# Performance work log

Hardware: AMD Instinct MI355X
Metric: run time of the kernel (lower is better)

Reference implementation:

```python
import math
import jax, jax.numpy as jnp
import numpy as np

N_HEADS, INPUT_DIM, EMBED_DIM = 8, 512, 512
KEY_DIM = EMBED_DIM // N_HEADS  # 64, val_dim == key_dim
BATCH, N = 4, 2048


def setup_inputs() -> dict:
    key = jax.random.key(0)
    ks = jax.random.split(key, 6)
    def unif(k, shape):
        stdv = 1.0 / math.sqrt(shape[-1])
        return jax.random.uniform(k, shape, jnp.float32, -stdv, stdv)
    q = jax.random.normal(ks[0], (BATCH, N, INPUT_DIM), jnp.float32)
    mask = jax.random.randint(ks[1], (BATCH, N, N), 0, 2, jnp.int32)
    W_query = unif(ks[2], (N_HEADS, INPUT_DIM, KEY_DIM))
    W_key = unif(ks[3], (N_HEADS, INPUT_DIM, KEY_DIM))
    W_val = unif(ks[4], (N_HEADS, INPUT_DIM, KEY_DIM))
    W_out = unif(ks[5], (N_HEADS, KEY_DIM, EMBED_DIM))
    return {"q": q, "mask": mask, "W_query": W_query, "W_key": W_key,
            "W_val": W_val, "W_out": W_out}


def reference(q, mask, W_query, W_key, W_val, W_out):
    # Self-attention: k is None, v is None -> k = q, v = q (module forward_).
    norm = 1.0 / math.sqrt(KEY_DIM)
    m = mask.astype(bool)[None]  # (1, b, nq, ng) broadcast over heads
    Q = jnp.einsum('bnd,hdk->hbnk', q, W_query)  # (h, b, nq, dk)
    K = jnp.einsum('bnd,hdk->hbnk', q, W_key)    # (h, b, ng, dk)
    V = jnp.einsum('bnd,hdv->hbnv', q, W_val)    # (h, b, ng, dv)
    scores = norm * jnp.einsum('hbqk,hbgk->hbqg', Q, K)  # (h, b, nq, ng)
    scores = jnp.where(m, -jnp.inf, scores)
    attn = jax.nn.softmax(scores, axis=-1)
    attn = jnp.where(m, 0.0, attn)  # zero out masked (also kills NaN rows)
    heads = jnp.einsum('hbqg,hbgv->hbqv', attn, V)
    out = jnp.einsum('hbqv,hve->bqe', heads, W_out)  # (b, nq, embed)
    return out
```

## Files before the change

### kernel.cpp

```cpp
#include <hip/hip_runtime.h>
#include <hip/hip_bf16.h>
#include <stdint.h>

using bf16 = __hip_bfloat16;
typedef __attribute__((ext_vector_type(8))) short short8;
typedef __attribute__((ext_vector_type(4))) short short4b;
typedef __attribute__((ext_vector_type(4))) float f32x4;
typedef __attribute__((ext_vector_type(4))) unsigned int u32x4;

#if __has_builtin(__builtin_amdgcn_exp2f)
#define EXP2(x) __builtin_amdgcn_exp2f(x)
#else
#define EXP2(x) exp2f(x)
#endif

__device__ __forceinline__ short8 load8(const bf16* p) {
  return *reinterpret_cast<const short8*>(p);
}
__device__ __forceinline__ short f2b(float f) {
  return __builtin_bit_cast(short, __float2bfloat16(f));
}
__device__ __forceinline__ unsigned int cvtpk(float lo, float hi) {
  unsigned int r;
  asm("v_cvt_pk_bf16_f32 %0, %1, %2" : "=v"(r) : "v"(lo), "v"(hi));
  return r;
}
__device__ __forceinline__ void asy16(const bf16* g, bf16* l) {
  __builtin_amdgcn_global_load_lds(
      (const __attribute__((address_space(1))) void*)g,
      (__attribute__((address_space(3))) void*)l, 16, 0, 0);
}


__global__ void k_prep(const float4* __restrict__ x, ushort4* __restrict__ xb,
                       const float* __restrict__ Wq, const float* __restrict__ Wk,
                       const float* __restrict__ Wv, const float* __restrict__ Wo,
                       bf16* __restrict__ Wcat, bf16* __restrict__ Wot,
                       const int4* __restrict__ m4,
                       unsigned long long* __restrict__ bits) {
  int blk = blockIdx.x;
  const int tid = threadIdx.x;
  if (blk < 4096) {
    int i = blk * 256 + tid;
    float4 v = x[i];
    ushort4 o;
    o.x = (unsigned short)f2b(v.x);
    o.y = (unsigned short)f2b(v.y);
    o.z = (unsigned short)f2b(v.z);
    o.w = (unsigned short)f2b(v.w);
    xb[i] = o;
  } else if (blk < 4352) {
    int t = blk - 4096;
    __shared__ float T[64][65];
    if (t < 192) {
      int which = t >> 6;
      int h = (t >> 3) & 7, dt = t & 7;
      const float* W = (which == 0) ? Wq : ((which == 1) ? Wk : Wv);
#pragma unroll
      for (int p = 0; p < 4; ++p) {
        int row = p * 16 + (tid >> 4);
        float4 v = *(const float4*)(W + (size_t)(h * 512 + dt * 64 + row) * 64 +
                                    (tid & 15) * 4);
        T[row][(tid & 15) * 4 + 0] = v.x;
        T[row][(tid & 15) * 4 + 1] = v.y;
        T[row][(tid & 15) * 4 + 2] = v.z;
        T[row][(tid & 15) * 4 + 3] = v.w;
      }
      __syncthreads();
      float scale = (which == 0) ? 0.18033688011112042f : 1.0f;
      int jj = tid >> 2, i0 = (tid & 3) * 16;
#pragma unroll
      for (int q = 0; q < 2; ++q) {
        short8 o;
#pragma unroll
        for (int e = 0; e < 8; ++e) o[e] = f2b(T[i0 + q * 8 + e][jj] * scale);
        *(short8*)(Wcat + (size_t)(which * 512 + h * 64 + jj) * 512 + dt * 64 +
                   i0 + q * 8) = o;
      }
    } else {
      int t2 = t - 192;
      int h = t2 >> 3, et = t2 & 7;
#pragma unroll
      for (int p = 0; p < 4; ++p) {
        int row = p * 16 + (tid >> 4);
        float4 v = *(const float4*)(Wo + (size_t)(h * 64 + row) * 512 + et * 64 +
                                    (tid & 15) * 4);
        T[row][(tid & 15) * 4 + 0] = v.x;
        T[row][(tid & 15) * 4 + 1] = v.y;
        T[row][(tid & 15) * 4 + 2] = v.z;
        T[row][(tid & 15) * 4 + 3] = v.w;
      }
      __syncthreads();
      int jj = tid >> 2, i0 = (tid & 3) * 16;
#pragma unroll
      for (int q = 0; q < 2; ++q) {
        short8 o;
#pragma unroll
        for (int e = 0; e < 8; ++e) o[e] = f2b(T[i0 + q * 8 + e][jj]);
        *(short8*)(Wot + (size_t)(et * 64 + jj) * 512 + h * 64 + i0 + q * 8) = o;
      }
    }
  } else {
    int i = (blk - 4352) * 256 + tid;
    int4 v = m4[i];
    unsigned int nib = (unsigned)(v.x != 0) | ((unsigned)(v.y != 0) << 1) |
                       ((unsigned)(v.z != 0) << 2) | ((unsigned)(v.w != 0) << 3);
    unsigned long long w = (unsigned long long)nib << (4 * (tid & 15));
    w |= __shfl_xor(w, 1);
    w |= __shfl_xor(w, 2);
    w |= __shfl_xor(w, 4);
    w |= __shfl_xor(w, 8);
    if ((tid & 15) == 0) bits[i >> 4] = w;
  }
}

__device__ __forceinline__ void gemm128(const bf16* __restrict__ A,
                                        const bf16* __restrict__ Bt,
                                        bf16* As, bf16* Bs,
                                        int rowBase, int colBase,
                                        f32x4 acc[4][4]) {
  const int tid = threadIdx.x;
  const int lane = tid & 63, w = tid >> 6;
  const int g = lane >> 4, r = lane & 15;

  auto stage = [&](int buf, int s) {
#pragma unroll
    for (int p = 0; p < 2; ++p) {
      int c = p * 256 + tid;
      int row = c >> 2, gr = c & 3, sg = gr ^ (row & 3);
      asy16(A + (size_t)(rowBase + row) * 512 + s * 32 + sg * 8,
            As + buf * 4096 + c * 8);
    }
#pragma unroll
    for (int p = 0; p < 2; ++p) {
      int c = p * 256 + tid;
      int row = c >> 2, gr = c & 3, sg = gr ^ (row & 3);
      asy16(Bt + (size_t)(colBase + row) * 512 + s * 32 + sg * 8,
            Bs + buf * 4096 + c * 8);
    }
  };

  stage(0, 0);
  int buf = 0;
  const int rbl = (w >> 1) * 64, cbl = (w & 1) * 64;
  for (int s = 0; s < 16; ++s) {
    __syncthreads();
    if (s < 15) stage(buf ^ 1, s + 1);
    const bf16* a0 = As + buf * 4096;
    const bf16* b0 = Bs + buf * 4096;
    short8 af[4], bfr[4];
#pragma unroll
    for (int mt = 0; mt < 4; ++mt) {
      int row = rbl + mt * 16 + r;
      af[mt] = load8(a0 + (row * 4 + (g ^ (row & 3))) * 8);
    }
#pragma unroll
    for (int nt = 0; nt < 4; ++nt) {
      int col = cbl + nt * 16 + r;
      bfr[nt] = load8(b0 + (col * 4 + (g ^ (col & 3))) * 8);
    }
#pragma unroll
    for (int mt = 0; mt < 4; ++mt)
#pragma unroll
      for (int nt = 0; nt < 4; ++nt)
        acc[mt][nt] = __builtin_amdgcn_mfma_f32_16x16x32_bf16(
            af[mt], bfr[nt], acc[mt][nt], 0, 0, 0);
    buf ^= 1;
  }
}

__device__ __forceinline__ void gemm64x128(const bf16* __restrict__ A,
                                           const bf16* __restrict__ Bt,
                                           bf16* As, bf16* Bs,
                                           int rowBase, int colBase,
                                           f32x4 acc[2][4]) {
  const int tid = threadIdx.x;
  const int lane = tid & 63, w = tid >> 6;
  const int g = lane >> 4, r = lane & 15;

  auto stage = [&](int buf, int s) {
    {
      int c = tid;
      int row = c >> 2, gr = c & 3, sg = gr ^ (row & 3);
      asy16(A + (size_t)(rowBase + row) * 512 + s * 32 + sg * 8,
            As + buf * 2048 + c * 8);
    }
#pragma unroll
    for (int p = 0; p < 2; ++p) {
      int c = p * 256 + tid;
      int row = c >> 2, gr = c & 3, sg = gr ^ (row & 3);
      asy16(Bt + (size_t)(colBase + row) * 512 + s * 32 + sg * 8,
            Bs + buf * 4096 + c * 8);
    }
  };

  stage(0, 0);
  int buf = 0;
  const int rbl = (w >> 1) * 32, cbl = (w & 1) * 64;
  for (int s = 0; s < 16; ++s) {
    __syncthreads();
    if (s < 15) stage(buf ^ 1, s + 1);
    const bf16* a0 = As + buf * 2048;
    const bf16* b0 = Bs + buf * 4096;
    short8 af[2], bfr[4];
#pragma unroll
    for (int mt = 0; mt < 2; ++mt) {
      int row = rbl + mt * 16 + r;
      af[mt] = load8(a0 + (row * 4 + (g ^ (row & 3))) * 8);
    }
#pragma unroll
    for (int nt = 0; nt < 4; ++nt) {
      int col = cbl + nt * 16 + r;
      bfr[nt] = load8(b0 + (col * 4 + (g ^ (col & 3))) * 8);
    }
#pragma unroll
    for (int mt = 0; mt < 2; ++mt)
#pragma unroll
      for (int nt = 0; nt < 4; ++nt)
        acc[mt][nt] = __builtin_amdgcn_mfma_f32_16x16x32_bf16(
            af[mt], bfr[nt], acc[mt][nt], 0, 0, 0);
    buf ^= 1;
  }
}

__global__ __launch_bounds__(256, 3) void k_proj_qkv(
    const bf16* __restrict__ Xb, const bf16* __restrict__ Wcat,
    bf16* __restrict__ Qb, bf16* __restrict__ Kp, bf16* __restrict__ Vp) {
  __shared__ __align__(16) bf16 As[2 * 4096];
  __shared__ __align__(16) bf16 Bs[2 * 4096];
  int rowBase = blockIdx.x * 128, colBase = blockIdx.y * 128;
  f32x4 acc[4][4] = {};
  gemm128(Xb, Wcat, As, Bs, rowBase, colBase, acc);
  const int lane = threadIdx.x & 63, w = threadIdx.x >> 6;
  const int g = lane >> 4, r = lane & 15;
#pragma unroll
  for (int mt = 0; mt < 4; ++mt) {
    int row0 = rowBase + (w >> 1) * 64 + mt * 16 + 4 * g;
    int b = row0 >> 11, n0 = row0 & 2047;
    int kt = n0 >> 6;
#pragma unroll
    for (int nt = 0; nt < 4; ++nt) {
      int col = colBase + (w & 1) * 64 + nt * 16 + r;
      if (col < 512) {
        int hh = col >> 6, dk = col & 63;
        bf16* p0 = Qb + ((size_t)(b * 8 + hh) * 2048 + n0) * 64 + dk;
#pragma unroll
        for (int rr = 0; rr < 4; ++rr)
          p0[rr * 64] = __float2bfloat16(acc[mt][nt][rr]);
      } else if (col < 1024) {
        int hh = (col >> 6) & 7, dk = col & 63;
        int half = dk >> 5, gk = (dk >> 3) & 3, jj = dk & 7;
        int kr = n0 & 63;
        int kc = kr >> 4, r0 = kr & 15;
        bf16* base = Kp + (size_t)(b * 8 + hh) * 131072 + (size_t)kt * 4096 +
                     ((kc * 2 + half) * 4 + gk) * 128 + jj;
#pragma unroll
        for (int rr = 0; rr < 4; ++rr)
          base[(r0 + rr) * 8] = __float2bfloat16(acc[mt][nt][rr]);
      } else {
        int hdv = col - 1024;
        int hh = hdv >> 6, dv = hdv & 63;
        int dvs = dv >> 4, rv = dv & 15;
        int kcol0 = n0 & 63;
        int half = kcol0 >> 5, gv = (kcol0 >> 2) & 3;
        int j0 = ((kcol0 >> 4) & 1) * 4;
        short4b pkv;
#pragma unroll
        for (int rr = 0; rr < 4; ++rr) pkv[rr] = f2b(acc[mt][nt][rr]);
        *reinterpret_cast<short4b*>(
            Vp + (size_t)(b * 8 + hh) * 131072 + (size_t)kt * 4096 +
            (((half * 4 + dvs) * 4 + gv) * 16 + rv) * 8 + j0) = pkv;
      }
    }
  }
}

__global__ __launch_bounds__(256, 4) void k_proj_out(
    const bf16* __restrict__ O, const bf16* __restrict__ Wot,
    float* __restrict__ out) {
  __shared__ __align__(16) bf16 As[2 * 2048];
  __shared__ __align__(16) bf16 Bs[2 * 4096];
  int rowBase = blockIdx.x * 64, colBase = blockIdx.y * 128;
  f32x4 acc[2][4] = {};
  gemm64x128(O, Wot, As, Bs, rowBase, colBase, acc);
  const int lane = threadIdx.x & 63, w = threadIdx.x >> 6;
  const int g = lane >> 4, r = lane & 15;
#pragma unroll
  for (int mt = 0; mt < 2; ++mt) {
    int row0 = rowBase + (w >> 1) * 32 + mt * 16 + 4 * g;
#pragma unroll
    for (int nt = 0; nt < 4; ++nt) {
      int col = colBase + (w & 1) * 64 + nt * 16 + r;
#pragma unroll
      for (int rr = 0; rr < 4; ++rr)
        out[(size_t)(row0 + rr) * 512 + col] = acc[mt][nt][rr];
    }
  }
}

__global__ __launch_bounds__(512, 4) void k_attn(const bf16* __restrict__ Q,
    const bf16* __restrict__ K, const bf16* __restrict__ V,
    const unsigned long long* __restrict__ MB, bf16* __restrict__ O) {
  const int blin = blockIdx.x;
  const int j = blin >> 3;
  const int bh = (blin & 7) * 4 + (j >> 4);
  const int qt = j & 15;
  const int b = bh >> 3, h = bh & 7;
  const int tid = threadIdx.x;
  const int lane = tid & 63;
  const int wave = tid >> 6;
  const int g = lane >> 4, r = lane & 15;
  const int qbase = qt * 128 + wave * 16;

  __shared__ __align__(16) bf16 Kl[3][4096];
  __shared__ __align__(16) bf16 Vl[3][4096];

  const bf16* Kp = K + (size_t)bh * 131072;
  const bf16* Vp = V + (size_t)bh * 131072;

  short8 qf0, qf1;
  {
    const bf16* Qp = Q + ((size_t)bh * 2048 + qbase + r) * 64;
    qf0 = load8(Qp + g * 8);
    qf1 = load8(Qp + 32 + g * 8);
  }
  const unsigned long long* Mp = MB + ((size_t)b * 2048 + qbase + r) * 32;

  short8 ones;
#pragma unroll
  for (int i = 0; i < 8; ++i) ones[i] = (short)0x3F80;

  f32x4 acc[4] = {};
  f32x4 acc_l = {};

  auto stage = [&](int buf, int kt) {
    const bf16* Kg = Kp + (size_t)kt * 4096;
    const bf16* Vg = Vp + (size_t)kt * 4096;
    asy16(Kg + tid * 8, &Kl[buf][0] + tid * 8);
    asy16(Vg + tid * 8, &Vl[buf][0] + tid * 8);
  };

  auto qk = [&](const bf16* kl, f32x4 stl[4]) {
#pragma unroll
    for (int kc = 0; kc < 4; ++kc) {
      short8 kf0 = load8(kl + ((kc * 2 + 0) * 4 + g) * 128 + r * 8);
      short8 kf1 = load8(kl + ((kc * 2 + 1) * 4 + g) * 128 + r * 8);
      f32x4 z = {};
      z = __builtin_amdgcn_mfma_f32_16x16x32_bf16(kf0, qf0, z, 0, 0, 0);
      stl[kc] = __builtin_amdgcn_mfma_f32_16x16x32_bf16(kf1, qf1, z, 0, 0, 0);
    }
  };

  stage(0, 0);
  stage(1, 1);
  unsigned long long mwc = Mp[0];
  __syncthreads();
  f32x4 st_cur[4];
  qk(&Kl[0][0], st_cur);

  int b_cur = 0, b_nxt = 1, b_st = 2;

  for (int kt = 0; kt < 32; ++kt) {
    __syncthreads();
    if (kt < 30) stage(b_st, kt + 2);
    unsigned long long mwn = 0;
    if (kt < 31) mwn = Mp[kt + 1];

    f32x4 stn[4];
    if (kt < 31) qk(&Kl[b_nxt][0], stn);

    unsigned ml = (unsigned)mwc >> (4 * g);
    unsigned mh = (unsigned)(mwc >> 32) >> (4 * g);
    float p[16];
#pragma unroll
    for (int kc = 0; kc < 4; ++kc)
#pragma unroll
      for (int rr = 0; rr < 4; ++rr) {
        float e = EXP2(st_cur[kc][rr]);
        unsigned wsel = (kc & 2) ? mh : ml;
        bool bad = (wsel >> (((kc & 1) << 4) + rr)) & 1u;
        p[kc * 4 + rr] = bad ? 0.f : e;
      }
    u32x4 q0, q1;
#pragma unroll
    for (int i2 = 0; i2 < 4; ++i2) {
      q0[i2] = cvtpk(p[2 * i2], p[2 * i2 + 1]);
      q1[i2] = cvtpk(p[8 + 2 * i2], p[8 + 2 * i2 + 1]);
    }
    short8 pa0 = __builtin_bit_cast(short8, q0);
    short8 pa1 = __builtin_bit_cast(short8, q1);
    acc_l = __builtin_amdgcn_mfma_f32_16x16x32_bf16(pa0, ones, acc_l, 0, 0, 0);
    acc_l = __builtin_amdgcn_mfma_f32_16x16x32_bf16(pa1, ones, acc_l, 0, 0, 0);

    const bf16* vl = &Vl[b_cur][0];
#pragma unroll
    for (int dvs = 0; dvs < 4; ++dvs) {
      short8 vb0 = load8(vl + ((0 * 4 + dvs) * 4 + g) * 128 + r * 8);
      short8 vb1 = load8(vl + ((1 * 4 + dvs) * 4 + g) * 128 + r * 8);
      acc[dvs] = __builtin_amdgcn_mfma_f32_16x16x32_bf16(pa0, vb0, acc[dvs], 0, 0, 0);
      acc[dvs] = __builtin_amdgcn_mfma_f32_16x16x32_bf16(pa1, vb1, acc[dvs], 0, 0, 0);
    }

#pragma unroll
    for (int kc = 0; kc < 4; ++kc) st_cur[kc] = stn[kc];
    mwc = mwn;
    int t = b_cur; b_cur = b_nxt; b_nxt = b_st; b_st = t;
  }

  float inv[4];
#pragma unroll
  for (int rr = 0; rr < 4; ++rr)
    inv[rr] = (acc_l[rr] > 0.f) ? 1.f / acc_l[rr] : 0.f;
  bf16* Op = O + ((size_t)b * 2048 + qbase + 4 * g) * 512 + h * 64;
#pragma unroll
  for (int dvs = 0; dvs < 4; ++dvs)
#pragma unroll
    for (int rr = 0; rr < 4; ++rr)
      Op[rr * 512 + dvs * 16 + r] = __float2bfloat16(acc[dvs][rr] * inv[rr]);
}


extern "C" void kernel_launch(void* const* d_in, const int* in_sizes, int n_in,
                              void* d_out, int out_size, void* d_ws, size_t ws_size,
                              hipStream_t stream) {
  const float* q    = (const float*)d_in[0];
  const int*   mask = (const int*)d_in[1];
  const float* Wq   = (const float*)d_in[2];
  const float* Wk   = (const float*)d_in[3];
  const float* Wv   = (const float*)d_in[4];
  const float* Wo   = (const float*)d_in[5];
  float* out = (float*)d_out;

  char* ws = (char*)d_ws;
  const size_t MB1 = 1024 * 1024;
  bf16* Xb   = (bf16*)(ws + 0);
  bf16* Ob   = (bf16*)(ws + 0);
  bf16* Qb   = (bf16*)(ws + 8 * MB1);
  bf16* Kpm  = (bf16*)(ws + 16 * MB1);
  bf16* Vpm  = (bf16*)(ws + 24 * MB1);
  unsigned long long* Mbits = (unsigned long long*)(ws + 32 * MB1);
  bf16* Wcat = (bf16*)(ws + 34 * MB1);
  bf16* Wot  = (bf16*)(ws + 34 * MB1 + 1536 * 512 * 2);

  k_prep<<<20736, 256, 0, stream>>>((const float4*)q, (ushort4*)Xb,
                                    Wq, Wk, Wv, Wo, Wcat, Wot,
                                    (const int4*)mask, Mbits);
  k_proj_qkv<<<dim3(64, 12), 256, 0, stream>>>(Xb, Wcat, Qb, Kpm, Vpm);
  k_attn<<<512, 512, 0, stream>>>(Qb, Kpm, Vpm, Mbits, Ob);
  k_proj_out<<<dim3(128, 4), 256, 0, stream>>>(Ob, Wot, out);
}
```

Measured before the change: 199.9 us.

## Restructure attention loop to double-buffer 128-key tiles, dropping cross-iteration QK pipelining

The K/V staging moves from a triple buffer of 64-key tiles to a double buffer of 128-key tiles, so the loop runs 16 iterations with one barrier each instead of 32. The mask words are fetched as 128-bit pairs. The software pipelining that computed the next tile's QK scores while the current tile's softmax·V ran is removed; both half-tiles now do QK then PV in sequence. The aim is to halve barrier and loop overhead. The cost is less QK/PV overlap inside a wave, and each iteration now depends on a larger async copy having landed. LDS use rises from 48KB to 64KB per block, which may limit occupancy.

```diff
diff --git a/kernel.cpp b/kernel.cpp
--- a/kernel.cpp
+++ b/kernel.cpp
@@ -312,8 +312,8 @@
   const int g = lane >> 4, r = lane & 15;
   const int qbase = qt * 128 + wave * 16;
 
-  __shared__ __align__(16) bf16 Kl[3][4096];
-  __shared__ __align__(16) bf16 Vl[3][4096];
+  __shared__ __align__(16) bf16 Kl[2][8192];
+  __shared__ __align__(16) bf16 Vl[2][8192];
 
   const bf16* Kp = K + (size_t)bh * 131072;
   const bf16* Vp = V + (size_t)bh * 131072;
@@ -333,11 +333,13 @@
   f32x4 acc[4] = {};
   f32x4 acc_l = {};
 
-  auto stage = [&](int buf, int kt) {
-    const bf16* Kg = Kp + (size_t)kt * 4096;
-    const bf16* Vg = Vp + (size_t)kt * 4096;
-    asy16(Kg + tid * 8, &Kl[buf][0] + tid * 8);
-    asy16(Vg + tid * 8, &Vl[buf][0] + tid * 8);
+  auto stageU = [&](int u, int t2) {
+    const bf16* Kg = Kp + (size_t)(2 * t2) * 4096;
+    const bf16* Vg = Vp + (size_t)(2 * t2) * 4096;
+    asy16(Kg + tid * 8, &Kl[u][0] + tid * 8);
+    asy16(Kg + 4096 + tid * 8, &Kl[u][0] + 4096 + tid * 8);
+    asy16(Vg + tid * 8, &Vl[u][0] + tid * 8);
+    asy16(Vg + 4096 + tid * 8, &Vl[u][0] + 4096 + tid * 8);
   };
 
   auto qk = [&](const bf16* kl, f32x4 stl[4]) {
@@ -351,32 +353,15 @@
     }
   };
 
-  stage(0, 0);
-  stage(1, 1);
-  unsigned long long mwc = Mp[0];
-  __syncthreads();
-  f32x4 st_cur[4];
-  qk(&Kl[0][0], st_cur);
-
-  int b_cur = 0, b_nxt = 1, b_st = 2;
-
-  for (int kt = 0; kt < 32; ++kt) {
-    __syncthreads();
-    if (kt < 30) stage(b_st, kt + 2);
-    unsigned long long mwn = 0;
-    if (kt < 31) mwn = Mp[kt + 1];
-
-    f32x4 stn[4];
-    if (kt < 31) qk(&Kl[b_nxt][0], stn);
-
-    unsigned ml = (unsigned)mwc >> (4 * g);
-    unsigned mh = (unsigned)(mwc >> 32) >> (4 * g);
+  auto smpv = [&](const f32x4 st[4], unsigned long long mw, const bf16* vl) {
+    unsigned ml = (unsigned)mw >> (4 * g);
+    unsigned mh = (unsigned)(mw >> 32) >> (4 * g);
     float p[16];
 #pragma unroll
     for (int kc = 0; kc < 4; ++kc)
 #pragma unroll
       for (int rr = 0; rr < 4; ++rr) {
-        float e = EXP2(st_cur[kc][rr]);
+        float e = EXP2(st[kc][rr]);
         unsigned wsel = (kc & 2) ? mh : ml;
         bool bad = (wsel >> (((kc & 1) << 4) + rr)) & 1u;
         p[kc * 4 + rr] = bad ? 0.f : e;
@@ -391,8 +376,6 @@
     short8 pa1 = __builtin_bit_cast(short8, q1);
     acc_l = __builtin_amdgcn_mfma_f32_16x16x32_bf16(pa0, ones, acc_l, 0, 0, 0);
     acc_l = __builtin_amdgcn_mfma_f32_16x16x32_bf16(pa1, ones, acc_l, 0, 0, 0);
-
-    const bf16* vl = &Vl[b_cur][0];
 #pragma unroll
     for (int dvs = 0; dvs < 4; ++dvs) {
       short8 vb0 = load8(vl + ((0 * 4 + dvs) * 4 + g) * 128 + r * 8);
@@ -400,11 +383,24 @@
       acc[dvs] = __builtin_amdgcn_mfma_f32_16x16x32_bf16(pa0, vb0, acc[dvs], 0, 0, 0);
       acc[dvs] = __builtin_amdgcn_mfma_f32_16x16x32_bf16(pa1, vb1, acc[dvs], 0, 0, 0);
     }
-
-#pragma unroll
-    for (int kc = 0; kc < 4; ++kc) st_cur[kc] = stn[kc];
-    mwc = mwn;
-    int t = b_cur; b_cur = b_nxt; b_nxt = b_st; b_st = t;
+  };
+
+  stageU(0, 0);
+  ulonglong2 mwp = *reinterpret_cast<const ulonglong2*>(Mp);
+
+  for (int t = 0; t < 16; ++t) {
+    const int u = t & 1;
+    __syncthreads();
+    if (t < 15) stageU(u ^ 1, t + 1);
+    unsigned long long mwa = mwp.x, mwb = mwp.y;
+    if (t < 15) mwp = *reinterpret_cast<const ulonglong2*>(Mp + 2 * (t + 1));
+
+    const bf16* kl = &Kl[u][0];
+    f32x4 sta[4], stb[4];
+    qk(kl, sta);
+    qk(kl + 4096, stb);
+    smpv(sta, mwa, &Vl[u][0]);
+    smpv(stb, mwb, &Vl[u][0] + 4096);
   }
 
   float inv[4];
```

New measurement: 201.9 us. No clear change (+1.0%).
